# Performance work log

Hardware: AMD Instinct MI355X
Metric: run time of the kernel (lower is better)

The kernel has to match this reference:

```python
import jax, jax.numpy as jnp
import numpy as np

B, S, H, E = 8, 512, 1024, 8
T = B * S            # total tokens
CAP = T // E         # capacity, capacity_factor = 1.0


def _moe(x, wg, ew1, eb1, ew2, eb2):
    # x: [T, H] tokens; top-1 gating with capacity, DeepSpeed-style dispatch/combine
    gates = jax.nn.softmax(x @ wg)                      # [T, E]
    idx = jnp.argmax(gates, axis=-1)                    # [T]
    mask1 = jax.nn.one_hot(idx, E, dtype=x.dtype)       # [T, E]
    locations = jnp.cumsum(mask1, axis=0) - 1.0         # position within expert queue
    mask1 = mask1 * (locations < CAP).astype(x.dtype)   # drop overflow tokens
    gates1 = jnp.sum(gates * mask1, axis=-1)            # [T] combine weight
    locs = jnp.sum(locations * mask1, axis=-1).astype(jnp.int32)  # [T]
    loc_oh = jax.nn.one_hot(locs, CAP, dtype=x.dtype)   # [T, C]
    combine = gates1[:, None, None] * mask1[:, :, None] * loc_oh[:, None, :]  # [T,E,C]
    dispatch = (combine > 0).astype(x.dtype)            # [T, E, C]
    xd = jnp.einsum('sec,sm->ecm', dispatch, x)         # gather tokens per expert
    h = jnp.einsum('ecm,emn->ecn', xd, ew1) + eb1[:, None, :]
    h = jnp.einsum('ecn,enp->ecp', h, ew2) + eb2[:, None, :]
    return jnp.einsum('sec,ecm->sm', combine, h)        # scatter back, weighted


def setup_inputs() -> dict:
    key = jax.random.key(0)
    ks = jax.random.split(key, 16)
    w = lambda k, shape: jax.random.normal(k, shape, jnp.float32) * 0.02
    return {
        'x': jax.random.normal(ks[0], (B, S, H), jnp.float32),
        'y': jax.random.randint(ks[1], (B,), 0, H),
        'w1': w(ks[2], (H, H)), 'b1': jnp.zeros((H,), jnp.float32),
        'w2': w(ks[3], (H, H)), 'b2': jnp.zeros((H,), jnp.float32),
        'w3': w(ks[4], (H, H)), 'b3': jnp.zeros((H,), jnp.float32),
        'wg1': w(ks[5], (H, E)),
        'e1_w1': w(ks[6], (E, H, H)), 'e1_b1': jnp.zeros((E, H), jnp.float32),
        'e1_w2': w(ks[7], (E, H, H)), 'e1_b2': jnp.zeros((E, H), jnp.float32),
        'wg2': w(ks[8], (H, E)),
        'e2_w1': w(ks[9], (E, H, H)), 'e2_b1': jnp.zeros((E, H), jnp.float32),
        'e2_w2': w(ks[10], (E, H, H)), 'e2_b2': jnp.zeros((E, H), jnp.float32),
    }


def reference(x, y, w1, b1, w2, b2, w3, b3, wg1, e1_w1, e1_b1, e1_w2, e1_b2,
              wg2, e2_w1, e2_b1, e2_w2, e2_b2):
    xf = x.reshape(-1, H)                               # [T, H]
    hidden = xf @ w1 + b1
    out = _moe(hidden, wg1, e1_w1, e1_b1, e1_w2, e1_b2)
    out = out @ w2 + b2
    out = _moe(out, wg2, e2_w1, e2_b1, e2_w2, e2_b2)
    out = out @ w3 + b3
    hidden = hidden + out
    sent = hidden.reshape(B, S, H).mean(axis=1)         # [B, H] logits
    logp = jax.nn.log_softmax(sent, axis=-1)
    return -jnp.mean(logp[jnp.arange(B), y])
```

## Files before the change

### kernel.cpp

```cpp
#include <hip/hip_runtime.h>

#define TOK 4096
#define HID 1024
#define NEXP 8
#define CAP 512
#define WSZ 1048576

typedef _Float16 f16;
typedef f16 f16x8 __attribute__((ext_vector_type(8)));
typedef f16 f16x4 __attribute__((ext_vector_type(4)));
typedef f16 f16x2 __attribute__((ext_vector_type(2)));
typedef float f32x4 __attribute__((ext_vector_type(4)));

typedef const __attribute__((address_space(1))) void gvoid;
typedef __attribute__((address_space(3))) void lvoid;

__device__ __forceinline__ void gld16(const void* g, void* l) {
  __builtin_amdgcn_global_load_lds((gvoid*)g, (lvoid*)l, 16, 0, 0);
}

template<int MODE>
__global__ __launch_bounds__(256, 2) void gemm_h(
    const f16* __restrict__ A, const f16* __restrict__ Bt,
    const float* __restrict__ bias, f16* __restrict__ C,
    const int* __restrict__ rowmap, const float* __restrict__ gmax,
    int rowsPerExpert, long bStride, int biasStride)
{
  __shared__ f16 As[2][64 * 64];
  __shared__ f16 Bs[2][128 * 64];
  const int tid = threadIdx.x;
  const int w = tid >> 6, l = tid & 63;

  const int orig = blockIdx.x;
  const int sw = (orig & 7) * 64 + (orig >> 3);
  const int bx = sw & 7, by = sw >> 3;
  const int e = (by * 64) / rowsPerExpert;

  const int lr = l >> 3;
  const int chunkSw = ((l & 7) ^ lr) * 8;

  const f16* pa[2];
  #pragma unroll
  for (int i = 0; i < 2; ++i) {
    int r = by * 64 + w * 16 + i * 8 + lr;
    long tok = r;
    if (MODE == 1) { int t = rowmap[r]; tok = (t < 0) ? (long)TOK : (long)t; }
    pa[i] = A + tok * HID + chunkSw;
  }
  const f16* pb = Bt + (size_t)e * bStride
                + (size_t)(bx * 128 + w * 32 + lr) * HID + chunkSw;

  f32x4 acc[4][2];
  #pragma unroll
  for (int i = 0; i < 4; ++i)
    #pragma unroll
    for (int j = 0; j < 2; ++j) acc[i][j] = (f32x4){0.f, 0.f, 0.f, 0.f};

  const int g = l >> 4, c = l & 15, sa = c & 7;

  {
    f16* ab = &As[0][(w * 16) * 64];
    f16* bb = &Bs[0][(w * 32) * 64];
    #pragma unroll
    for (int i = 0; i < 2; ++i) gld16(pa[i], ab + i * 8 * 64);
    #pragma unroll
    for (int i = 0; i < 4; ++i) gld16(pb + (size_t)(i * 8) * HID, bb + i * 8 * 64);
  }

  int cur = 0;
  for (int t = 0; t < 15; ++t) {
    {
      const int k0 = (t + 1) * 64;
      f16* ab = &As[cur ^ 1][(w * 16) * 64];
      f16* bb = &Bs[cur ^ 1][(w * 32) * 64];
      #pragma unroll
      for (int i = 0; i < 2; ++i) gld16(pa[i] + k0, ab + i * 8 * 64);
      #pragma unroll
      for (int i = 0; i < 4; ++i) gld16(pb + (size_t)(i * 8) * HID + k0, bb + i * 8 * 64);
    }
    asm volatile("s_waitcnt vmcnt(6)" ::: "memory");
    asm volatile("s_barrier" ::: "memory");
    __builtin_amdgcn_s_setprio(1);
    #pragma unroll
    for (int h = 0; h < 2; ++h) {
      const int q = ((h * 4 + g) ^ sa) * 8;
      f16x8 af[4], bf[2];
      #pragma unroll
      for (int mi = 0; mi < 4; ++mi)
        af[mi] = *(const f16x8*)&As[cur][(mi * 16 + c) * 64 + q];
      #pragma unroll
      for (int ni = 0; ni < 2; ++ni)
        bf[ni] = *(const f16x8*)&Bs[cur][(w * 32 + ni * 16 + c) * 64 + q];
      #pragma unroll
      for (int mi = 0; mi < 4; ++mi)
        #pragma unroll
        for (int ni = 0; ni < 2; ++ni)
          acc[mi][ni] = __builtin_amdgcn_mfma_f32_16x16x32_f16(
              af[mi], bf[ni], acc[mi][ni], 0, 0, 0);
    }
    __builtin_amdgcn_s_setprio(0);
    asm volatile("s_barrier" ::: "memory");
    cur ^= 1;
  }
  asm volatile("s_waitcnt vmcnt(0)" ::: "memory");
  asm volatile("s_barrier" ::: "memory");
  #pragma unroll
  for (int h = 0; h < 2; ++h) {
    const int q = ((h * 4 + g) ^ sa) * 8;
    f16x8 af[4], bf[2];
    #pragma unroll
    for (int mi = 0; mi < 4; ++mi)
      af[mi] = *(const f16x8*)&As[cur][(mi * 16 + c) * 64 + q];
    #pragma unroll
    for (int ni = 0; ni < 2; ++ni)
      bf[ni] = *(const f16x8*)&Bs[cur][(w * 32 + ni * 16 + c) * 64 + q];
    #pragma unroll
    for (int mi = 0; mi < 4; ++mi)
      #pragma unroll
      for (int ni = 0; ni < 2; ++ni)
        acc[mi][ni] = __builtin_amdgcn_mfma_f32_16x16x32_f16(
            af[mi], bf[ni], acc[mi][ni], 0, 0, 0);
  }

  int tk[4][4];
  float gv[4][4];
  if (MODE == 2) {
    #pragma unroll
    for (int mi = 0; mi < 4; ++mi)
      #pragma unroll
      for (int rr = 0; rr < 4; ++rr) {
        int r = by * 64 + mi * 16 + g * 4 + rr;
        int t = rowmap[r];
        tk[mi][rr] = t;
        gv[mi][rr] = (t >= 0) ? gmax[t] : 0.f;
      }
  }
  #pragma unroll
  for (int ni = 0; ni < 2; ++ni) {
    const int col = bx * 128 + w * 32 + ni * 16 + c;
    const float bv = bias[(size_t)e * biasStride + col];
    #pragma unroll
    for (int mi = 0; mi < 4; ++mi) {
      #pragma unroll
      for (int rr = 0; rr < 4; ++rr) {
        const float v = acc[mi][ni][rr] + bv;
        if (MODE == 2) {
          if (tk[mi][rr] >= 0)
            C[(size_t)tk[mi][rr] * HID + col] = (f16)(v * gv[mi][rr]);
        } else {
          const int row = by * 64 + mi * 16 + g * 4 + rr;
          C[(size_t)row * HID + col] = (f16)v;
        }
      }
    }
  }
}

__global__ __launch_bounds__(256) void tcast(
    const float* __restrict__ w1, const float* __restrict__ w2,
    const float* __restrict__ w3,
    const float* __restrict__ g1a, const float* __restrict__ g1b,
    const float* __restrict__ g2a, const float* __restrict__ g2b,
    f16* __restrict__ dst)
{
  __shared__ float t[64][129];
  const int z = blockIdx.z;
  const float* src; int zl = 0;
  if (z == 0) src = w1;
  else if (z == 1) src = w2;
  else if (z == 2) src = w3;
  else if (z < 11) { src = g1a; zl = z - 3; }
  else if (z < 19) { src = g1b; zl = z - 11; }
  else if (z < 27) { src = g2a; zl = z - 19; }
  else             { src = g2b; zl = z - 27; }
  src += (size_t)zl * WSZ;
  f16* d = dst + (size_t)z * WSZ;

  const int tid = threadIdx.x;
  const int kb = blockIdx.y * 64, nb = blockIdx.x * 128;
  const int r = (tid >> 4) & 3, half = tid >> 6, c4 = (tid & 15) * 4;
  float4 v[8];
  #pragma unroll
  for (int p = 0; p < 8; ++p)
    v[p] = *(const float4*)&src[(size_t)(kb + p * 8 + half * 4 + r) * HID
                                + nb + c4 + (tid & 256 ? 0 : 0)];
  #pragma unroll
  for (int p = 0; p < 8; ++p) {
    const int row = p * 8 + (tid >> 6) * 2 + (r >> 1);
  }
  __syncthreads();
  {
    const int rr = tid >> 4, cc4 = (tid & 15) * 4;
    #pragma unroll
    for (int p = 0; p < 4; ++p) {
      #pragma unroll
      for (int hf = 0; hf < 2; ++hf) {
        float4 vv = *(const float4*)&src[(size_t)(kb + p * 16 + rr) * HID
                                         + nb + hf * 64 + cc4];
        t[p * 16 + rr][hf * 64 + cc4 + 0] = vv.x;
        t[p * 16 + rr][hf * 64 + cc4 + 1] = vv.y;
        t[p * 16 + rr][hf * 64 + cc4 + 2] = vv.z;
        t[p * 16 + rr][hf * 64 + cc4 + 3] = vv.w;
      }
    }
  }
  __syncthreads();
  #pragma unroll
  for (int it = 0; it < 4; ++it) {
    const int p = it * 256 + tid;
    const int n = p >> 3, kc = p & 7;
    f16x8 o;
    #pragma unroll
    for (int j = 0; j < 8; ++j) o[j] = (f16)t[kc * 8 + j][n];
    *(f16x8*)&d[(size_t)(nb + n) * HID + kb + kc * 8] = o;
  }
}

__global__ void prep(const float* __restrict__ x, f16* __restrict__ X0,
                     f16* __restrict__ c1, f16* __restrict__ c2,
                     f16* __restrict__ p1, f16* __restrict__ p2) {
  const size_t i = (size_t)blockIdx.x * 256 + threadIdx.x;
  float4 v = *(const float4*)&x[i * 4];
  f16x4 o = {(f16)v.x, (f16)v.y, (f16)v.z, (f16)v.w};
  *(f16x4*)&X0[i * 4] = o;
  const f16x8 zz = {0, 0, 0, 0, 0, 0, 0, 0};
  if (i < 524288) { ((f16x8*)c1)[i] = zz; ((f16x8*)c2)[i] = zz; }
  if (i < 128)    { ((f16x8*)p1)[i] = zz; ((f16x8*)p2)[i] = zz; }
}

__global__ __launch_bounds__(256) void gate_kernel(
    const f16* __restrict__ act, const float* __restrict__ wg,
    int* __restrict__ idx, float* __restrict__ gmax)
{
  const int tid = threadIdx.x;
  const int tok = blockIdx.x * 8 + (tid >> 5);
  const int sl = tid & 31;
  const f16* row = act + (size_t)tok * HID + sl * 32;
  float xv[32];
  #pragma unroll
  for (int v = 0; v < 4; ++v) {
    f16x8 hv = *(const f16x8*)(row + v * 8);
    #pragma unroll
    for (int j = 0; j < 8; ++j) xv[v * 8 + j] = (float)hv[j];
  }
  float p[NEXP];
  #pragma unroll
  for (int e = 0; e < NEXP; ++e) p[e] = 0.f;
  const float* wr_ = wg + (size_t)(sl * 32) * NEXP;
  #pragma unroll
  for (int j = 0; j < 32; ++j) {
    #pragma unroll
    for (int e = 0; e < NEXP; ++e) p[e] += xv[j] * wr_[j * NEXP + e];
  }
  #pragma unroll
  for (int m = 1; m < 32; m <<= 1) {
    #pragma unroll
    for (int e = 0; e < NEXP; ++e) p[e] += __shfl_xor(p[e], m, 64);
  }
  if (sl == 0) {
    float mx = p[0]; int am = 0;
    #pragma unroll
    for (int e = 1; e < NEXP; ++e)
      if (p[e] > mx) { mx = p[e]; am = e; }
    float s = 0.f;
    #pragma unroll
    for (int e = 0; e < NEXP; ++e) s += expf(p[e] - mx);
    idx[tok] = am;
    gmax[tok] = 1.f / s;
  }
}

__global__ __launch_bounds__(512) void scan_kernel(
    const int* __restrict__ idx, int* __restrict__ rowmap)
{
  __shared__ int sidx[TOK];
  const int tid = threadIdx.x;
  for (int i = tid; i < TOK; i += 512) sidx[i] = idx[i];
  for (int i = tid; i < NEXP * CAP; i += 512) rowmap[i] = -1;
  __syncthreads();
  const int wave = tid >> 6, lane = tid & 63;
  int running = 0;
  for (int ch = 0; ch < TOK / 64; ++ch) {
    int t = ch * 64 + lane;
    bool flag = (sidx[t] == wave);
    unsigned long long m = __ballot(flag);
    int pos = running + __popcll(m & ((1ull << lane) - 1ull));
    if (flag && pos < CAP) rowmap[wave * CAP + pos] = t;
    running += __popcll(m);
  }
}

__global__ __launch_bounds__(256) void mean_kernel(
    const f16* __restrict__ a, const f16* __restrict__ c,
    float* __restrict__ sent)
{
  const int h2 = blockIdx.x * 256 + threadIdx.x;
  const int b = blockIdx.y;
  const f16x2* pa = (const f16x2*)(a + (size_t)b * 512 * HID) + h2;
  const f16x2* pc = (const f16x2*)(c + (size_t)b * 512 * HID) + h2;
  float a0 = 0.f, a1 = 0.f;
  for (int s = 0; s < 512; ++s) {
    f16x2 va = pa[(size_t)s * 512];
    f16x2 vc = pc[(size_t)s * 512];
    a0 += (float)va[0] + (float)vc[0];
    a1 += (float)va[1] + (float)vc[1];
  }
  sent[b * HID + h2 * 2]     = a0 * (1.f / 512.f);
  sent[b * HID + h2 * 2 + 1] = a1 * (1.f / 512.f);
}

__global__ __launch_bounds__(1024) void loss_kernel(
    const float* __restrict__ sent, const int* __restrict__ y,
    float* __restrict__ out)
{
  __shared__ float red[1024];
  float loss = 0.0f;
  for (int b = 0; b < 8; ++b) {
    float v = sent[b * HID + threadIdx.x];
    red[threadIdx.x] = v;
    __syncthreads();
    for (int s = 512; s > 0; s >>= 1) {
      if (threadIdx.x < s)
        red[threadIdx.x] = fmaxf(red[threadIdx.x], red[threadIdx.x + s]);
      __syncthreads();
    }
    float m = red[0];
    __syncthreads();
    red[threadIdx.x] = expf(v - m);
    __syncthreads();
    for (int s = 512; s > 0; s >>= 1) {
      if (threadIdx.x < s) red[threadIdx.x] += red[threadIdx.x + s];
      __syncthreads();
    }
    if (threadIdx.x == 0) {
      float lse = m + logf(red[0]);
      loss += -(sent[b * HID + y[b]] - lse);
    }
    __syncthreads();
  }
  if (threadIdx.x == 0) out[0] = loss * (1.0f / 8.0f);
}

extern "C" void kernel_launch(void* const* d_in, const int* in_sizes, int n_in,
                              void* d_out, int out_size, void* d_ws, size_t ws_size,
                              hipStream_t stream)
{
  const float* x    = (const float*)d_in[0];
  const int*   y    = (const int*)d_in[1];
  const float* w1   = (const float*)d_in[2];
  const float* b1   = (const float*)d_in[3];
  const float* w2   = (const float*)d_in[4];
  const float* b2   = (const float*)d_in[5];
  const float* w3   = (const float*)d_in[6];
  const float* b3   = (const float*)d_in[7];
  const float* wg1  = (const float*)d_in[8];
  const float* e1w1 = (const float*)d_in[9];
  const float* e1b1 = (const float*)d_in[10];
  const float* e1w2 = (const float*)d_in[11];
  const float* e1b2 = (const float*)d_in[12];
  const float* wg2  = (const float*)d_in[13];
  const float* e2w1 = (const float*)d_in[14];
  const float* e2b1 = (const float*)d_in[15];
  const float* e2w2 = (const float*)d_in[16];
  const float* e2b2 = (const float*)d_in[17];

  f16* WT = (f16*)d_ws;
  f16* X0 = WT + (size_t)35 * WSZ;
  f16* H  = X0 + (size_t)TOK * HID;
  f16* EA = H + (size_t)(TOK + 1) * HID;
  f16* C1 = EA + (size_t)TOK * HID;
  f16* M1 = C1 + (size_t)TOK * HID;
  f16* C2 = M1 + (size_t)(TOK + 1) * HID;
  f16* O  = C2 + (size_t)TOK * HID;
  float* gmax  = (float*)(O + (size_t)TOK * HID);
  int* idx     = (int*)(gmax + TOK);
  int* rowmap  = idx + TOK;
  float* sent  = (float*)(rowmap + TOK);

  prep<<<4096, 256, 0, stream>>>(x, X0, C1, C2,
                                 H + (size_t)TOK * HID, M1 + (size_t)TOK * HID);
  tcast<<<dim3(8, 16, 35), 256, 0, stream>>>(w1, w2, w3, e1w1, e1w2, e2w1, e2w2, WT);

  gemm_h<0><<<512, 256, 0, stream>>>(X0, WT, b1, H, nullptr, nullptr, TOK, 0, 0);

  gate_kernel<<<512, 256, 0, stream>>>(H, wg1, idx, gmax);
  scan_kernel<<<1, 512, 0, stream>>>(idx, rowmap);
  gemm_h<1><<<512, 256, 0, stream>>>(H,  WT + (size_t)3 * WSZ,  e1b1, EA, rowmap, nullptr, CAP, WSZ, HID);
  gemm_h<2><<<512, 256, 0, stream>>>(EA, WT + (size_t)11 * WSZ, e1b2, C1, rowmap, gmax,    CAP, WSZ, HID);

  gemm_h<0><<<512, 256, 0, stream>>>(C1, WT + (size_t)1 * WSZ, b2, M1, nullptr, nullptr, TOK, 0, 0);

  gate_kernel<<<512, 256, 0, stream>>>(M1, wg2, idx, gmax);
  scan_kernel<<<1, 512, 0, stream>>>(idx, rowmap);
  gemm_h<1><<<512, 256, 0, stream>>>(M1, WT + (size_t)19 * WSZ, e2b1, EA, rowmap, nullptr, CAP, WSZ, HID);
  gemm_h<2><<<512, 256, 0, stream>>>(EA, WT + (size_t)27 * WSZ, e2b2, C2, rowmap, gmax,    CAP, WSZ, HID);

  gemm_h<0><<<512, 256, 0, stream>>>(C2, WT + (size_t)2 * WSZ, b3, O, nullptr, nullptr, TOK, 0, 0);

  mean_kernel<<<dim3(2, 8), 256, 0, stream>>>(H, O, sent);
  loss_kernel<<<1, 1024, 0, stream>>>(sent, y, (float*)d_out);
}
```

Before: 263.0 us.

## Enlarge GEMM tiles to 128x128, simplify transpose-cast, split mean reduction

The GEMM moves from a 64x128 tile with 256 threads to a 128x128 tile with 512 threads. Waves 0-3 now load A and waves 4-7 load B, and each wave computes a 64x32 sub-tile, so every staged byte is reused across more outputs. The tcast kernel drops its dead first pass that loaded the source twice and uses 64x64 tiles. The serial 512-step mean becomes a two-stage parallel reduction over 16 sequence chunks, fixing a launch with only 16 blocks. The risks are fewer blocks for the GEMM (256 on a large GPU, one per CU) and higher LDS and register use per block.

```diff
diff --git a/kernel.cpp b/kernel.cpp
--- a/kernel.cpp
+++ b/kernel.cpp
@@ -20,35 +20,41 @@
 }
 
 template<int MODE>
-__global__ __launch_bounds__(256, 2) void gemm_h(
+__global__ __launch_bounds__(512, 1) void gemm_h(
     const f16* __restrict__ A, const f16* __restrict__ Bt,
     const float* __restrict__ bias, f16* __restrict__ C,
     const int* __restrict__ rowmap, const float* __restrict__ gmax,
     int rowsPerExpert, long bStride, int biasStride)
 {
-  __shared__ f16 As[2][64 * 64];
+  __shared__ f16 As[2][128 * 64];
   __shared__ f16 Bs[2][128 * 64];
   const int tid = threadIdx.x;
   const int w = tid >> 6, l = tid & 63;
+  const int wr = w >> 2, wc = w & 3;
 
   const int orig = blockIdx.x;
-  const int sw = (orig & 7) * 64 + (orig >> 3);
+  const int sw = (orig & 7) * 32 + (orig >> 3);
   const int bx = sw & 7, by = sw >> 3;
-  const int e = (by * 64) / rowsPerExpert;
+  const int e = (by * 128) / rowsPerExpert;
 
   const int lr = l >> 3;
   const int chunkSw = ((l & 7) ^ lr) * 8;
 
-  const f16* pa[2];
-  #pragma unroll
-  for (int i = 0; i < 2; ++i) {
-    int r = by * 64 + w * 16 + i * 8 + lr;
-    long tok = r;
-    if (MODE == 1) { int t = rowmap[r]; tok = (t < 0) ? (long)TOK : (long)t; }
-    pa[i] = A + tok * HID + chunkSw;
-  }
-  const f16* pb = Bt + (size_t)e * bStride
-                + (size_t)(bx * 128 + w * 32 + lr) * HID + chunkSw;
+  const f16* pst[4];
+  if (w < 4) {
+    #pragma unroll
+    for (int i = 0; i < 4; ++i) {
+      int r = by * 128 + w * 32 + i * 8 + lr;
+      long tok = r;
+      if (MODE == 1) { int t = rowmap[r]; tok = (t < 0) ? (long)TOK : (long)t; }
+      pst[i] = A + tok * HID + chunkSw;
+    }
+  } else {
+    #pragma unroll
+    for (int i = 0; i < 4; ++i)
+      pst[i] = Bt + (size_t)e * bStride
+             + (size_t)(bx * 128 + (w - 4) * 32 + i * 8 + lr) * HID + chunkSw;
+  }
 
   f32x4 acc[4][2];
   #pragma unroll
@@ -59,26 +65,21 @@
   const int g = l >> 4, c = l & 15, sa = c & 7;
 
   {
-    f16* ab = &As[0][(w * 16) * 64];
-    f16* bb = &Bs[0][(w * 32) * 64];
-    #pragma unroll
-    for (int i = 0; i < 2; ++i) gld16(pa[i], ab + i * 8 * 64);
-    #pragma unroll
-    for (int i = 0; i < 4; ++i) gld16(pb + (size_t)(i * 8) * HID, bb + i * 8 * 64);
+    f16* db = (w < 4) ? &As[0][(w * 32) * 64] : &Bs[0][((w - 4) * 32) * 64];
+    #pragma unroll
+    for (int i = 0; i < 4; ++i) gld16(pst[i], db + i * 8 * 64);
   }
 
   int cur = 0;
   for (int t = 0; t < 15; ++t) {
     {
       const int k0 = (t + 1) * 64;
-      f16* ab = &As[cur ^ 1][(w * 16) * 64];
-      f16* bb = &Bs[cur ^ 1][(w * 32) * 64];
-      #pragma unroll
-      for (int i = 0; i < 2; ++i) gld16(pa[i] + k0, ab + i * 8 * 64);
-      #pragma unroll
-      for (int i = 0; i < 4; ++i) gld16(pb + (size_t)(i * 8) * HID + k0, bb + i * 8 * 64);
-    }
-    asm volatile("s_waitcnt vmcnt(6)" ::: "memory");
+      f16* db = (w < 4) ? &As[cur ^ 1][(w * 32) * 64]
+                        : &Bs[cur ^ 1][((w - 4) * 32) * 64];
+      #pragma unroll
+      for (int i = 0; i < 4; ++i) gld16(pst[i] + k0, db + i * 8 * 64);
+    }
+    asm volatile("s_waitcnt vmcnt(4)" ::: "memory");
     asm volatile("s_barrier" ::: "memory");
     __builtin_amdgcn_s_setprio(1);
     #pragma unroll
@@ -87,10 +88,10 @@
       f16x8 af[4], bf[2];
       #pragma unroll
       for (int mi = 0; mi < 4; ++mi)
-        af[mi] = *(const f16x8*)&As[cur][(mi * 16 + c) * 64 + q];
+        af[mi] = *(const f16x8*)&As[cur][(wr * 64 + mi * 16 + c) * 64 + q];
       #pragma unroll
       for (int ni = 0; ni < 2; ++ni)
-        bf[ni] = *(const f16x8*)&Bs[cur][(w * 32 + ni * 16 + c) * 64 + q];
+        bf[ni] = *(const f16x8*)&Bs[cur][(wc * 32 + ni * 16 + c) * 64 + q];
       #pragma unroll
       for (int mi = 0; mi < 4; ++mi)
         #pragma unroll
@@ -110,10 +111,10 @@
     f16x8 af[4], bf[2];
     #pragma unroll
     for (int mi = 0; mi < 4; ++mi)
-      af[mi] = *(const f16x8*)&As[cur][(mi * 16 + c) * 64 + q];
+      af[mi] = *(const f16x8*)&As[cur][(wr * 64 + mi * 16 + c) * 64 + q];
     #pragma unroll
     for (int ni = 0; ni < 2; ++ni)
-      bf[ni] = *(const f16x8*)&Bs[cur][(w * 32 + ni * 16 + c) * 64 + q];
+      bf[ni] = *(const f16x8*)&Bs[cur][(wc * 32 + ni * 16 + c) * 64 + q];
     #pragma unroll
     for (int mi = 0; mi < 4; ++mi)
       #pragma unroll
@@ -129,7 +130,7 @@
     for (int mi = 0; mi < 4; ++mi)
       #pragma unroll
       for (int rr = 0; rr < 4; ++rr) {
-        int r = by * 64 + mi * 16 + g * 4 + rr;
+        int r = by * 128 + wr * 64 + mi * 16 + g * 4 + rr;
         int t = rowmap[r];
         tk[mi][rr] = t;
         gv[mi][rr] = (t >= 0) ? gmax[t] : 0.f;
@@ -137,7 +138,7 @@
   }
   #pragma unroll
   for (int ni = 0; ni < 2; ++ni) {
-    const int col = bx * 128 + w * 32 + ni * 16 + c;
+    const int col = bx * 128 + wc * 32 + ni * 16 + c;
     const float bv = bias[(size_t)e * biasStride + col];
     #pragma unroll
     for (int mi = 0; mi < 4; ++mi) {
@@ -148,7 +149,7 @@
           if (tk[mi][rr] >= 0)
             C[(size_t)tk[mi][rr] * HID + col] = (f16)(v * gv[mi][rr]);
         } else {
-          const int row = by * 64 + mi * 16 + g * 4 + rr;
+          const int row = by * 128 + wr * 64 + mi * 16 + g * 4 + rr;
           C[(size_t)row * HID + col] = (f16)v;
         }
       }
@@ -156,14 +157,14 @@
   }
 }
 
-__global__ __launch_bounds__(256) void tcast(
+__global__ __launch_bounds__(256, 8) void tcast(
     const float* __restrict__ w1, const float* __restrict__ w2,
     const float* __restrict__ w3,
     const float* __restrict__ g1a, const float* __restrict__ g1b,
     const float* __restrict__ g2a, const float* __restrict__ g2b,
     f16* __restrict__ dst)
 {
-  __shared__ float t[64][129];
+  __shared__ float t[64][65];
   const int z = blockIdx.z;
   const float* src; int zl = 0;
   if (z == 0) src = w1;
@@ -177,37 +178,23 @@
   f16* d = dst + (size_t)z * WSZ;
 
   const int tid = threadIdx.x;
-  const int kb = blockIdx.y * 64, nb = blockIdx.x * 128;
-  const int r = (tid >> 4) & 3, half = tid >> 6, c4 = (tid & 15) * 4;
-  float4 v[8];
-  #pragma unroll
-  for (int p = 0; p < 8; ++p)
-    v[p] = *(const float4*)&src[(size_t)(kb + p * 8 + half * 4 + r) * HID
-                                + nb + c4 + (tid & 256 ? 0 : 0)];
-  #pragma unroll
-  for (int p = 0; p < 8; ++p) {
-    const int row = p * 8 + (tid >> 6) * 2 + (r >> 1);
+  const int kb = blockIdx.y * 64, nb = blockIdx.x * 64;
+  const int rr = tid >> 4, c4 = (tid & 15) * 4;
+  float4 v[4];
+  #pragma unroll
+  for (int p = 0; p < 4; ++p)
+    v[p] = *(const float4*)&src[(size_t)(kb + p * 16 + rr) * HID + nb + c4];
+  #pragma unroll
+  for (int p = 0; p < 4; ++p) {
+    t[p * 16 + rr][c4 + 0] = v[p].x;
+    t[p * 16 + rr][c4 + 1] = v[p].y;
+    t[p * 16 + rr][c4 + 2] = v[p].z;
+    t[p * 16 + rr][c4 + 3] = v[p].w;
   }
   __syncthreads();
-  {
-    const int rr = tid >> 4, cc4 = (tid & 15) * 4;
-    #pragma unroll
-    for (int p = 0; p < 4; ++p) {
-      #pragma unroll
-      for (int hf = 0; hf < 2; ++hf) {
-        float4 vv = *(const float4*)&src[(size_t)(kb + p * 16 + rr) * HID
-                                         + nb + hf * 64 + cc4];
-        t[p * 16 + rr][hf * 64 + cc4 + 0] = vv.x;
-        t[p * 16 + rr][hf * 64 + cc4 + 1] = vv.y;
-        t[p * 16 + rr][hf * 64 + cc4 + 2] = vv.z;
-        t[p * 16 + rr][hf * 64 + cc4 + 3] = vv.w;
-      }
-    }
-  }
-  __syncthreads();
-  #pragma unroll
-  for (int it = 0; it < 4; ++it) {
-    const int p = it * 256 + tid;
+  #pragma unroll
+  for (int half = 0; half < 2; ++half) {
+    const int p = half * 256 + tid;
     const int n = p >> 3, kc = p & 7;
     f16x8 o;
     #pragma unroll
@@ -290,20 +277,37 @@
   }
 }
 
-__global__ __launch_bounds__(256) void mean_kernel(
+__global__ __launch_bounds__(256) void mean1_kernel(
     const f16* __restrict__ a, const f16* __restrict__ c,
-    float* __restrict__ sent)
+    float* __restrict__ partial)
 {
   const int h2 = blockIdx.x * 256 + threadIdx.x;
-  const int b = blockIdx.y;
-  const f16x2* pa = (const f16x2*)(a + (size_t)b * 512 * HID) + h2;
-  const f16x2* pc = (const f16x2*)(c + (size_t)b * 512 * HID) + h2;
+  const int b = blockIdx.y, sc = blockIdx.z;
+  const f16x2* pa = (const f16x2*)(a + ((size_t)b * 512 + sc * 32) * HID) + h2;
+  const f16x2* pc = (const f16x2*)(c + ((size_t)b * 512 + sc * 32) * HID) + h2;
   float a0 = 0.f, a1 = 0.f;
-  for (int s = 0; s < 512; ++s) {
+  #pragma unroll 4
+  for (int s = 0; s < 32; ++s) {
     f16x2 va = pa[(size_t)s * 512];
     f16x2 vc = pc[(size_t)s * 512];
     a0 += (float)va[0] + (float)vc[0];
     a1 += (float)va[1] + (float)vc[1];
+  }
+  float* o = partial + ((size_t)sc * 8 + b) * HID;
+  o[h2 * 2]     = a0;
+  o[h2 * 2 + 1] = a1;
+}
+
+__global__ __launch_bounds__(256) void mean2_kernel(
+    const float* __restrict__ partial, float* __restrict__ sent)
+{
+  const int h2 = blockIdx.x * 256 + threadIdx.x;
+  const int b = blockIdx.y;
+  float a0 = 0.f, a1 = 0.f;
+  #pragma unroll
+  for (int sc = 0; sc < 16; ++sc) {
+    const float* p = partial + ((size_t)sc * 8 + b) * HID + h2 * 2;
+    a0 += p[0]; a1 += p[1];
   }
   sent[b * HID + h2 * 2]     = a0 * (1.f / 512.f);
   sent[b * HID + h2 * 2 + 1] = a1 * (1.f / 512.f);
@@ -376,27 +380,29 @@
   int* idx     = (int*)(gmax + TOK);
   int* rowmap  = idx + TOK;
   float* sent  = (float*)(rowmap + TOK);
+  float* partial = sent + 8 * HID;
 
   prep<<<4096, 256, 0, stream>>>(x, X0, C1, C2,
                                  H + (size_t)TOK * HID, M1 + (size_t)TOK * HID);
-  tcast<<<dim3(8, 16, 35), 256, 0, stream>>>(w1, w2, w3, e1w1, e1w2, e2w1, e2w2, WT);
-
-  gemm_h<0><<<512, 256, 0, stream>>>(X0, WT, b1, H, nullptr, nullptr, TOK, 0, 0);
+  tcast<<<dim3(16, 16, 35), 256, 0, stream>>>(w1, w2, w3, e1w1, e1w2, e2w1, e2w2, WT);
+
+  gemm_h<0><<<256, 512, 0, stream>>>(X0, WT, b1, H, nullptr, nullptr, TOK, 0, 0);
 
   gate_kernel<<<512, 256, 0, stream>>>(H, wg1, idx, gmax);
   scan_kernel<<<1, 512, 0, stream>>>(idx, rowmap);
-  gemm_h<1><<<512, 256, 0, stream>>>(H,  WT + (size_t)3 * WSZ,  e1b1, EA, rowmap, nullptr, CAP, WSZ, HID);
-  gemm_h<2><<<512, 256, 0, stream>>>(EA, WT + (size_t)11 * WSZ, e1b2, C1, rowmap, gmax,    CAP, WSZ, HID);
-
-  gemm_h<0><<<512, 256, 0, stream>>>(C1, WT + (size_t)1 * WSZ, b2, M1, nullptr, nullptr, TOK, 0, 0);
+  gemm_h<1><<<256, 512, 0, stream>>>(H,  WT + (size_t)3 * WSZ,  e1b1, EA, rowmap, nullptr, CAP, WSZ, HID);
+  gemm_h<2><<<256, 512, 0, stream>>>(EA, WT + (size_t)11 * WSZ, e1b2, C1, rowmap, gmax,    CAP, WSZ, HID);
+
+  gemm_h<0><<<256, 512, 0, stream>>>(C1, WT + (size_t)1 * WSZ, b2, M1, nullptr, nullptr, TOK, 0, 0);
 
   gate_kernel<<<512, 256, 0, stream>>>(M1, wg2, idx, gmax);
   scan_kernel<<<1, 512, 0, stream>>>(idx, rowmap);
-  gemm_h<1><<<512, 256, 0, stream>>>(M1, WT + (size_t)19 * WSZ, e2b1, EA, rowmap, nullptr, CAP, WSZ, HID);
-  gemm_h<2><<<512, 256, 0, stream>>>(EA, WT + (size_t)27 * WSZ, e2b2, C2, rowmap, gmax,    CAP, WSZ, HID);
-
-  gemm_h<0><<<512, 256, 0, stream>>>(C2, WT + (size_t)2 * WSZ, b3, O, nullptr, nullptr, TOK, 0, 0);
-
-  mean_kernel<<<dim3(2, 8), 256, 0, stream>>>(H, O, sent);
+  gemm_h<1><<<256, 512, 0, stream>>>(M1, WT + (size_t)19 * WSZ, e2b1, EA, rowmap, nullptr, CAP, WSZ, HID);
+  gemm_h<2><<<256, 512, 0, stream>>>(EA, WT + (size_t)27 * WSZ, e2b2, C2, rowmap, gmax,    CAP, WSZ, HID);
+
+  gemm_h<0><<<256, 512, 0, stream>>>(C2, WT + (size_t)2 * WSZ, b3, O, nullptr, nullptr, TOK, 0, 0);
+
+  mean1_kernel<<<dim3(2, 8, 16), 256, 0, stream>>>(H, O, partial);
+  mean2_kernel<<<dim3(2, 8), 256, 0, stream>>>(partial, sent);
   loss_kernel<<<1, 1024, 0, stream>>>(sent, y, (float*)d_out);
 }
```

Result: faster. 229.0 us (-12.9%).
